# Kernel tuning notes

Measured on AMD Instinct MI355X. Metric: run time of the kernel, lower is better.

The kernel has to match this reference:

```python
import jax, jax.numpy as jnp
import numpy as np

N_HEADS = 16
HEAD_SIZE = 64
N_EMB = 1024
BLOCK = 2048
B, T = 2, 2048

def setup_inputs() -> dict:
    key = jax.random.key(0)
    ks = jax.random.split(key, 6)
    s = 0.02
    x = jax.random.normal(ks[0], (B, T, N_EMB), dtype=jnp.float32)
    # per-head projection weights, stacked: [H, C, hs] (no bias, per module)
    Wq = jax.random.normal(ks[1], (N_HEADS, N_EMB, HEAD_SIZE), dtype=jnp.float32) * s
    Wk = jax.random.normal(ks[2], (N_HEADS, N_EMB, HEAD_SIZE), dtype=jnp.float32) * s
    Wv = jax.random.normal(ks[3], (N_HEADS, N_EMB, HEAD_SIZE), dtype=jnp.float32) * s
    # output projection: Linear(n_heads*head_size -> n_embedding), with bias
    Wo = jax.random.normal(ks[4], (N_HEADS * HEAD_SIZE, N_EMB), dtype=jnp.float32) * s
    bo = jax.random.normal(ks[5], (N_EMB,), dtype=jnp.float32) * s
    return {"x": x, "Wq": Wq, "Wk": Wk, "Wv": Wv, "Wo": Wo, "bo": bo}

def reference(x, Wq, Wk, Wv, Wo, bo):
    # x: [B,T,C]; projections per head -> [B,H,T,hs]
    q = jnp.einsum('btc,hcd->bhtd', x, Wq)
    k = jnp.einsum('btc,hcd->bhtd', x, Wk)
    v = jnp.einsum('btc,hcd->bhtd', x, Wv)
    scale = 1.0 / jnp.sqrt(jnp.asarray(HEAD_SIZE, dtype=x.dtype))
    scores = jnp.einsum('bhtd,bhsd->bhts', q, k) * scale  # [B,H,T,T]
    Tq = x.shape[1]
    causal = jnp.tril(jnp.ones((Tq, Tq), dtype=bool))
    scores = jnp.where(causal, scores, jnp.asarray(-jnp.inf, dtype=scores.dtype))
    attn = jax.nn.softmax(scores, axis=-1)  # dropout in eval mode (identity)
    out = jnp.einsum('bhts,bhsd->bhtd', attn, v)  # [B,H,T,hs]
    # concat heads along last dim (matches torch.cat order over head list)
    out = out.transpose(0, 2, 1, 3).reshape(x.shape[0], Tq, N_HEADS * HEAD_SIZE)
    return out @ Wo + bo
```

## Files before the change

### kernel.cpp

```cpp
#include <hip/hip_runtime.h>


typedef short v8s __attribute__((ext_vector_type(8)));
typedef float v4f __attribute__((ext_vector_type(4)));

#define DEVI __device__ __forceinline__

#define B_SZ 2
#define T_SEQ 2048
#define NH 16
#define HS 64
#define CEMB 1024
#define MROWS (B_SZ * T_SEQ)
#define KSZ 1024
#define SCALE_Q 0.18033688011112042f

DEVI unsigned short f2bf(float f) {
  union { float f; unsigned u; } c; c.f = f;
  unsigned u = c.u;
  unsigned r = (u + 0x7FFFu + ((u >> 16) & 1u)) >> 16;
  return (unsigned short)r;
}

DEVI float exp2_fast(float x) {
  float r;
  asm("v_exp_f32 %0, %1" : "=v"(r) : "v"(x));
  return r;
}

DEVI unsigned cvt_pk_bf16(float lo, float hi) {
  unsigned r;
  asm("v_cvt_pk_bf16_f32 %0, %1, %2" : "=v"(r) : "v"(lo), "v"(hi));
  return r;
}

DEVI void gload_lds16(const void* g, void* l) {
  __builtin_amdgcn_global_load_lds(
      (const __attribute__((address_space(1))) void*)g,
      (__attribute__((address_space(3))) void*)l, 16, 0, 0);
}

DEVI int xcd_swz(int bid, int nwg) {
  int q = nwg >> 3;
  return (bid & 7) * q + (bid >> 3);
}

__global__ __launch_bounds__(256, 4) void prep_kernel(
    const float* __restrict__ x, const float* __restrict__ Wq,
    const float* __restrict__ Wk, const float* __restrict__ Wv,
    const float* __restrict__ Wo, unsigned short* __restrict__ xb,
    unsigned short* __restrict__ Wt, unsigned short* __restrict__ Wot) {
  int bid = blockIdx.x;
  if (bid < 2048) {
    int i = bid * 2048 + threadIdx.x * 8;
    float4 a = *(const float4*)(x + i);
    float4 b = *(const float4*)(x + i + 4);
    ushort4 o0, o1;
    o0.x = f2bf(a.x); o0.y = f2bf(a.y); o0.z = f2bf(a.z); o0.w = f2bf(a.w);
    o1.x = f2bf(b.x); o1.y = f2bf(b.y); o1.z = f2bf(b.z); o1.w = f2bf(b.w);
    *(ushort4*)(xb + i) = o0;
    *(ushort4*)(xb + i + 4) = o1;
    return;
  }
  __shared__ float tile[32][33];
  const float* in; unsigned short* out;
  int C, bx, by;
  if (bid < 5120) {
    int b2 = bid - 2048;
    int widx = b2 >> 10, rem = b2 & 1023;
    in = (widx == 0 ? Wq : (widx == 1 ? Wk : Wv));
    int z = rem >> 6;
    bx = rem & 1; by = (rem >> 1) & 31;
    C = 64;
    in += (size_t)z * 1024 * 64;
    out = Wt + ((size_t)widx << 20) + (size_t)z * 1024 * 64;
  } else {
    int rem = bid - 5120;
    C = 1024;
    bx = rem & 31; by = rem >> 5;
    in = Wo; out = Wot;
  }
  int c0 = bx * 32, r0 = by * 32;
  int tx = threadIdx.x & 31, ty = threadIdx.x >> 5;
#pragma unroll
  for (int j = 0; j < 4; ++j)
    tile[ty + j * 8][tx] = in[(size_t)(r0 + ty + j * 8) * C + c0 + tx];
  __syncthreads();
#pragma unroll
  for (int j = 0; j < 4; ++j)
    out[(size_t)(c0 + ty + j * 8) * 1024 + r0 + tx] = f2bf(tile[tx][ty + j * 8]);
}

template <int MODE>
__global__ __launch_bounds__(256, 3) void gemm_bt(
    const unsigned short* __restrict__ A, const unsigned short* __restrict__ Bt,
    void* __restrict__ Cout, const float* __restrict__ bias, int nbx) {
  __shared__ __align__(16) unsigned char lds[49152];
  unsigned short* As = (unsigned short*)lds;
  unsigned short* Bs = (unsigned short*)(lds + 24576);

  const int tid = threadIdx.x;
  const int lane = tid & 63, w = tid >> 6;
  const int wm = w >> 1, wn = w & 1;
  const int lr = lane & 15, lg = lane >> 4;

  const int wg = xcd_swz(blockIdx.x, gridDim.x);
  const int mb = (wg / nbx) * 128, nb = (wg % nbx) * 128;

  v4f acc[4][4];
  v4f zero = {0.f, 0.f, 0.f, 0.f};
#pragma unroll
  for (int i = 0; i < 4; ++i)
#pragma unroll
    for (int j = 0; j < 4; ++j) acc[i][j] = zero;

  const int srow = lane >> 2;
  const int sgcol = ((lane & 3) ^ (srow & 3)) * 8;
  const unsigned short* gA = A + (size_t)(mb + w * 32 + srow) * KSZ + sgcol;
  const unsigned short* gB = Bt + (size_t)(nb + w * 32 + srow) * KSZ + sgcol;
  unsigned short* lA = As + w * 1024;
  unsigned short* lB = Bs + w * 1024;

#define STAGE_G(buf, kb)                                        \
  do {                                                          \
    gload_lds16(gA + (kb), lA + (buf) * 4096);                  \
    gload_lds16(gA + (kb) + 16 * KSZ, lA + (buf) * 4096 + 512); \
    gload_lds16(gB + (kb), lB + (buf) * 4096);                  \
    gload_lds16(gB + (kb) + 16 * KSZ, lB + (buf) * 4096 + 512); \
  } while (0)

  STAGE_G(0, 0);
  STAGE_G(1, 32);
  STAGE_G(2, 64);

  const int NT = KSZ / 32;
  for (int t = 0; t < NT; ++t) {
    if (t < NT - 2)
      asm volatile("s_waitcnt vmcnt(8)" ::: "memory");
    else if (t == NT - 2)
      asm volatile("s_waitcnt vmcnt(4)" ::: "memory");
    else
      asm volatile("s_waitcnt vmcnt(0)" ::: "memory");
    __builtin_amdgcn_s_barrier();

    const int buf = t % 3;
    v8s af[4], bfr[4];
#pragma unroll
    for (int i = 0; i < 4; ++i) {
      int ra = wm * 64 + i * 16 + lr, rb = wn * 64 + i * 16 + lr;
      af[i]  = *(const v8s*)&As[buf * 4096 + ra * 32 + ((lg ^ (lr & 3)) << 3)];
      bfr[i] = *(const v8s*)&Bs[buf * 4096 + rb * 32 + ((lg ^ (lr & 3)) << 3)];
    }
#pragma unroll
    for (int i = 0; i < 4; ++i)
#pragma unroll
      for (int j = 0; j < 4; ++j)
        acc[i][j] = __builtin_amdgcn_mfma_f32_16x16x32_bf16(af[i], bfr[j], acc[i][j], 0, 0, 0);

    asm volatile("s_waitcnt lgkmcnt(0)" ::: "memory");
    __builtin_amdgcn_s_barrier();
    if (t + 3 < NT) STAGE_G(buf, (t + 3) * 32);
  }
#undef STAGE_G

  if (MODE == 0 && (wg % nbx) >= 16) {
    unsigned short* out = (unsigned short*)Cout;
#pragma unroll
    for (int i = 0; i < 4; ++i) {
      int tl0 = wm * 64 + i * 16 + lg * 4;
      int tc = tl0 >> 3, off = (tl0 & 7) * 2;
#pragma unroll
      for (int j = 0; j < 4; ++j) {
        int dl = wn * 64 + j * 16 + lr;
        unsigned lo = cvt_pk_bf16(acc[i][j][0], acc[i][j][1]);
        unsigned hi = cvt_pk_bf16(acc[i][j][2], acc[i][j][3]);
        unsigned char* p = lds + dl * 256 + ((tc ^ (dl & 15)) << 4) + off;
        *(unsigned*)p = lo;
        *(unsigned*)(p + 4) = hi;
      }
    }
    __syncthreads();
    int b = mb >> 11, mt = mb & 2047;
    int nrem0 = nb & 1023;
    unsigned short* Vg = out + (size_t)(2 * B_SZ * NH) * T_SEQ * HS;
#pragma unroll
    for (int it = 0; it < 8; ++it) {
      int dl = it * 16 + (tid >> 4);
      int tc = tid & 15;
      const unsigned char* p = lds + dl * 256 + ((tc ^ (dl & 15)) << 4);
      int4 vv = *(const int4*)p;
      int nrem = nrem0 + dl;
      int h = nrem >> 6, dd = nrem & 63;
      *(int4*)(Vg + ((size_t)(b * NH + h) * HS + dd) * T_SEQ + mt + tc * 8) = vv;
    }
    return;
  }

#pragma unroll
  for (int i = 0; i < 4; ++i) {
    int mrow0 = mb + wm * 64 + i * 16 + lg * 4;
#pragma unroll
    for (int j = 0; j < 4; ++j) {
      int ncol = nb + wn * 64 + j * 16 + lr;
      if (MODE == 0) {
        int p = ncol >> 10, rem = ncol & 1023, h = rem >> 6, d = rem & 63;
        float sc = (p == 0) ? SCALE_Q : 1.0f;
        unsigned short* out = (unsigned short*)Cout;
#pragma unroll
        for (int r = 0; r < 4; ++r) {
          int mrow = mrow0 + r;
          int b = mrow >> 11, t = mrow & 2047;
          out[((size_t)((p * B_SZ + b) * NH + h) * T_SEQ + t) * HS + d] =
              f2bf(acc[i][j][r] * sc);
        }
      } else {
        float* out = (float*)Cout;
        float bv = bias[ncol];
#pragma unroll
        for (int r = 0; r < 4; ++r)
          out[(size_t)(mrow0 + r) * CEMB + ncol] = acc[i][j][r] + bv;
      }
    }
  }
}

__global__ __launch_bounds__(512, 4) void attn_kernel(
    const unsigned short* __restrict__ Qg, const unsigned short* __restrict__ Kg,
    const unsigned short* __restrict__ Vtg, unsigned short* __restrict__ Yg) {
  __shared__ __align__(16) unsigned char lds[32 * 1024];
  unsigned char* KsB = lds;
  unsigned char* VtB = lds + 16384;

  const int tid = threadIdx.x;
  const int lane = tid & 63, w = tid >> 6;
  const int lr = lane & 15, lg = lane >> 4;
  const int qc = 15 - (blockIdx.x >> 5);
  const int bh = blockIdx.x & 31;

  const unsigned short* Qbase = Qg + (size_t)bh * T_SEQ * HS;
  const unsigned short* Kbase = Kg + (size_t)bh * T_SEQ * HS;
  const unsigned short* Vtbase = Vtg + (size_t)bh * T_SEQ * HS;

  const int ks_row = tid >> 3, ks_cb = tid & 7;
  const int kLds0 = ks_row * 128 + ((ks_cb ^ (ks_row & 7)) << 4);
  const unsigned short* Kg0 = Kbase + ks_row * HS + ks_cb * 8;
  const int vs_d = tid >> 4, vs_m = tid & 15;
  const int vLds0 = vs_d * 256 + ((vs_m ^ (vs_d & 15)) << 4);
  const int vbt = ((vs_m >> 2) << 4) + ((vs_m & 3) << 2);
  const unsigned short* Vg0 = Vtbase + (size_t)vs_d * T_SEQ + vbt;

  v8s qA[2];
  {
    const unsigned short* qrow = Qbase + (size_t)(qc * 128 + w * 16 + lr) * HS;
    qA[0] = *(const v8s*)(qrow + lg * 8);
    qA[1] = *(const v8s*)(qrow + 32 + lg * 8);
  }

  v4f O[4];
  v4f zero = {0.f, 0.f, 0.f, 0.f};
#pragma unroll
  for (int d = 0; d < 4; ++d) O[d] = zero;
  float mrun = -1e30f, lrun = 0.f;

  int4 gK0 = *(const int4*)(Kg0);
  int4 gK1 = *(const int4*)(Kg0 + 4096);
  int2 vlo0 = *(const int2*)(Vg0);
  int2 vhi0 = *(const int2*)(Vg0 + 64);
  int2 vlo1 = *(const int2*)(Vg0 + 32 * T_SEQ);
  int2 vhi1 = *(const int2*)(Vg0 + 32 * T_SEQ + 64);

  for (int t = 0; t <= qc; ++t) {
    __syncthreads();
    *(int4*)(KsB + kLds0) = gK0;
    *(int4*)(KsB + kLds0 + 8192) = gK1;
    {
      int4 v0; v0.x = vlo0.x; v0.y = vlo0.y; v0.z = vhi0.x; v0.w = vhi0.y;
      int4 v1; v1.x = vlo1.x; v1.y = vlo1.y; v1.z = vhi1.x; v1.w = vhi1.y;
      *(int4*)(VtB + vLds0) = v0;
      *(int4*)(VtB + vLds0 + 8192) = v1;
    }
    __syncthreads();
    if (t < qc) {
      const unsigned short* kp = Kg0 + (t + 1) * (128 * HS);
      gK0 = *(const int4*)kp;
      gK1 = *(const int4*)(kp + 4096);
      const unsigned short* vp = Vg0 + (t + 1) * 128;
      vlo0 = *(const int2*)(vp);
      vhi0 = *(const int2*)(vp + 64);
      vlo1 = *(const int2*)(vp + 32 * T_SEQ);
      vhi1 = *(const int2*)(vp + 32 * T_SEQ + 64);
    }

    const int cflim = (t == qc) ? w : 7;

    v4f S[8];
    __builtin_amdgcn_s_setprio(1);
#pragma unroll
    for (int cf = 0; cf < 8; ++cf) {
      if (cf <= cflim) {
        S[cf] = zero;
#pragma unroll
        for (int ks = 0; ks < 2; ++ks) {
          int srow = cf * 16 + lr;
          v8s kb = *(const v8s*)(KsB + srow * 128 +
                                 ((((ks << 2) + lg) ^ (lr & 7)) << 4));
          S[cf] = __builtin_amdgcn_mfma_f32_16x16x32_bf16(kb, qA[ks], S[cf], 0, 0, 0);
        }
      } else {
        S[cf] = (v4f){-1e30f, -1e30f, -1e30f, -1e30f};
      }
    }
    __builtin_amdgcn_s_setprio(0);

    if (t == qc) {
#pragma unroll
      for (int cf = 0; cf < 8; ++cf)
        if (cf == w) {
#pragma unroll
          for (int r = 0; r < 4; ++r)
            if (lg * 4 + r > lr) S[cf][r] = -1e30f;
        }
    }

    float mx = -1e30f;
#pragma unroll
    for (int cf = 0; cf < 8; ++cf)
#pragma unroll
      for (int r = 0; r < 4; ++r) mx = fmaxf(mx, S[cf][r]);
    mx = fmaxf(mx, __shfl_xor(mx, 16));
    mx = fmaxf(mx, __shfl_xor(mx, 32));

    if (!__all(mx - mrun <= 8.0f)) {
      float mn = fmaxf(mrun, mx);
      float alpha = exp2_fast(mrun - mn);
      mrun = mn;
      lrun *= alpha;
#pragma unroll
      for (int df = 0; df < 4; ++df)
#pragma unroll
        for (int r = 0; r < 4; ++r) O[df][r] *= alpha;
    }

    float sum = 0.f;
#pragma unroll
    for (int cf = 0; cf < 8; ++cf)
#pragma unroll
      for (int r = 0; r < 4; ++r) {
        float p = exp2_fast(S[cf][r] - mrun);
        S[cf][r] = p;
        sum += p;
      }
    sum += __shfl_xor(sum, 16);
    sum += __shfl_xor(sum, 32);
    lrun += sum;

    unsigned pk0[8], pk1[8];
#pragma unroll
    for (int cf = 0; cf < 8; ++cf) {
      pk0[cf] = cvt_pk_bf16(S[cf][0], S[cf][1]);
      pk1[cf] = cvt_pk_bf16(S[cf][2], S[cf][3]);
    }

    __builtin_amdgcn_s_setprio(1);
#pragma unroll
    for (int c = 0; c < 4; ++c) {
      if (t != qc || c <= w) {
        union { unsigned u[4]; v8s s; } pu;
        pu.u[0] = pk0[c]; pu.u[1] = pk1[c];
        pu.u[2] = pk0[c + 4]; pu.u[3] = pk1[c + 4];
        v8s pa = pu.s;
#pragma unroll
        for (int df = 0; df < 4; ++df) {
          int d = df * 16 + lr;
          v8s va = *(const v8s*)(VtB + d * 256 +
                                 ((((c << 2) + lg) ^ lr) << 4));
          O[df] = __builtin_amdgcn_mfma_f32_16x16x32_bf16(va, pa, O[df], 0, 0, 0);
        }
      }
    }
    __builtin_amdgcn_s_setprio(0);
  }

  float invl = 1.0f / lrun;
  int tq = qc * 128 + w * 16 + lr;
  int b = bh >> 4, h = bh & 15;
  size_t ybase = ((size_t)b * T_SEQ + tq) * (NH * HS) + h * 64;
#pragma unroll
  for (int df = 0; df < 4; ++df) {
    ushort4 o4;
    o4.x = f2bf(O[df][0] * invl);
    o4.y = f2bf(O[df][1] * invl);
    o4.z = f2bf(O[df][2] * invl);
    o4.w = f2bf(O[df][3] * invl);
    *(ushort4*)(Yg + ybase + df * 16 + lg * 4) = o4;
  }
}

extern "C" void kernel_launch(void* const* d_in, const int* in_sizes, int n_in,
                              void* d_out, int out_size, void* d_ws, size_t ws_size,
                              hipStream_t stream) {
  (void)in_sizes; (void)n_in; (void)out_size; (void)ws_size;
  const float* x  = (const float*)d_in[0];
  const float* Wq = (const float*)d_in[1];
  const float* Wk = (const float*)d_in[2];
  const float* Wv = (const float*)d_in[3];
  const float* Wo = (const float*)d_in[4];
  const float* bo = (const float*)d_in[5];

  unsigned char* ws = (unsigned char*)d_ws;
  unsigned short* xb  = (unsigned short*)(ws);
  unsigned short* Wt  = (unsigned short*)(ws + (8u << 20));
  unsigned short* Wot = (unsigned short*)(ws + (14u << 20));
  unsigned short* qkv = (unsigned short*)(ws + (16u << 20));
  unsigned short* Y   = (unsigned short*)(ws + (40u << 20));

  prep_kernel<<<dim3(6144), 256, 0, stream>>>(x, Wq, Wk, Wv, Wo, xb, Wt, Wot);

  gemm_bt<0><<<dim3(768), 256, 0, stream>>>(xb, Wt, qkv, nullptr, 24);

  const unsigned short* Qp = qkv;
  const unsigned short* Kp = qkv + (size_t)B_SZ * NH * T_SEQ * HS;
  const unsigned short* Vtp = qkv + (size_t)2 * B_SZ * NH * T_SEQ * HS;
  attn_kernel<<<dim3(512), 512, 0, stream>>>(Qp, Kp, Vtp, Y);

  gemm_bt<1><<<dim3(256), 256, 0, stream>>>(Y, Wot, d_out, bo, 8);
}
```

Before: 99.49 us.

## Halve attention query tile and output-projection M tile to raise block count

Attention now uses 64-row query chunks with 256-thread blocks (1024 blocks instead of 512), staging 128-key K/V tiles with wider per-thread loads and handling the diagonal partially for odd chunks. The output projection GEMM gets its own kernel with 64x128 tiles, launching 512 blocks instead of 256, with a smaller triple-buffered LDS footprint. The aim is more concurrent blocks and better load balance across the CUs. The cost is more redundant K/V reloads per query row and lower per-block MFMA reuse.

Result: slower. 111.5 us (+12.1%).

```diff
diff --git a/kernel.cpp b/kernel.cpp
--- a/kernel.cpp
+++ b/kernel.cpp
@@ -91,10 +91,9 @@
     out[(size_t)(c0 + ty + j * 8) * 1024 + r0 + tx] = f2bf(tile[tx][ty + j * 8]);
 }
 
-template <int MODE>
-__global__ __launch_bounds__(256, 3) void gemm_bt(
+__global__ __launch_bounds__(256, 3) void gemm_qkv(
     const unsigned short* __restrict__ A, const unsigned short* __restrict__ Bt,
-    void* __restrict__ Cout, const float* __restrict__ bias, int nbx) {
+    unsigned short* __restrict__ Cout, int nbx) {
   __shared__ __align__(16) unsigned char lds[49152];
   unsigned short* As = (unsigned short*)lds;
   unsigned short* Bs = (unsigned short*)(lds + 24576);
@@ -163,7 +162,7 @@
   }
 #undef STAGE_G
 
-  if (MODE == 0 && (wg % nbx) >= 16) {
+  if ((wg % nbx) >= 16) {
     unsigned short* out = (unsigned short*)Cout;
 #pragma unroll
     for (int i = 0; i < 4; ++i) {
@@ -202,29 +201,108 @@
 #pragma unroll
     for (int j = 0; j < 4; ++j) {
       int ncol = nb + wn * 64 + j * 16 + lr;
-      if (MODE == 0) {
-        int p = ncol >> 10, rem = ncol & 1023, h = rem >> 6, d = rem & 63;
-        float sc = (p == 0) ? SCALE_Q : 1.0f;
-        unsigned short* out = (unsigned short*)Cout;
-#pragma unroll
-        for (int r = 0; r < 4; ++r) {
-          int mrow = mrow0 + r;
-          int b = mrow >> 11, t = mrow & 2047;
-          out[((size_t)((p * B_SZ + b) * NH + h) * T_SEQ + t) * HS + d] =
-              f2bf(acc[i][j][r] * sc);
-        }
-      } else {
-        float* out = (float*)Cout;
-        float bv = bias[ncol];
-#pragma unroll
-        for (int r = 0; r < 4; ++r)
-          out[(size_t)(mrow0 + r) * CEMB + ncol] = acc[i][j][r] + bv;
+      int p = ncol >> 10, rem = ncol & 1023, h = rem >> 6, d = rem & 63;
+      float sc = (p == 0) ? SCALE_Q : 1.0f;
+      unsigned short* out = (unsigned short*)Cout;
+#pragma unroll
+      for (int r = 0; r < 4; ++r) {
+        int mrow = mrow0 + r;
+        int b = mrow >> 11, t = mrow & 2047;
+        out[((size_t)((p * B_SZ + b) * NH + h) * T_SEQ + t) * HS + d] =
+            f2bf(acc[i][j][r] * sc);
       }
     }
   }
 }
 
-__global__ __launch_bounds__(512, 4) void attn_kernel(
+__global__ __launch_bounds__(256, 4) void gemm_proj(
+    const unsigned short* __restrict__ A, const unsigned short* __restrict__ Bt,
+    float* __restrict__ Cout, const float* __restrict__ bias, int nbx) {
+  __shared__ __align__(16) unsigned short As[3][64 * 32];
+  __shared__ __align__(16) unsigned short Bs[3][128 * 32];
+
+  const int tid = threadIdx.x;
+  const int lane = tid & 63, w = tid >> 6;
+  const int wm = w >> 1, wn = w & 1;
+  const int lr = lane & 15, lg = lane >> 4;
+
+  const int wg = xcd_swz(blockIdx.x, gridDim.x);
+  const int mb = (wg / nbx) * 64, nb = (wg % nbx) * 128;
+
+  v4f acc[2][4];
+  v4f zero = {0.f, 0.f, 0.f, 0.f};
+#pragma unroll
+  for (int i = 0; i < 2; ++i)
+#pragma unroll
+    for (int j = 0; j < 4; ++j) acc[i][j] = zero;
+
+  const int srow = lane >> 2;
+  const int sgcol = ((lane & 3) ^ (srow & 3)) * 8;
+  const unsigned short* gA = A + (size_t)(mb + w * 16 + srow) * KSZ + sgcol;
+  const unsigned short* gB = Bt + (size_t)(nb + w * 32 + srow) * KSZ + sgcol;
+  unsigned short* lA = &As[0][0] + w * 512;
+  unsigned short* lB = &Bs[0][0] + w * 1024;
+
+#define STAGE_P(buf, kb)                                        \
+  do {                                                          \
+    gload_lds16(gA + (kb), lA + (buf) * 2048);                  \
+    gload_lds16(gB + (kb), lB + (buf) * 4096);                  \
+    gload_lds16(gB + (kb) + 16 * KSZ, lB + (buf) * 4096 + 512); \
+  } while (0)
+
+  STAGE_P(0, 0);
+  STAGE_P(1, 32);
+  STAGE_P(2, 64);
+
+  const int NT = KSZ / 32;
+  for (int t = 0; t < NT; ++t) {
+    if (t < NT - 2)
+      asm volatile("s_waitcnt vmcnt(6)" ::: "memory");
+    else if (t == NT - 2)
+      asm volatile("s_waitcnt vmcnt(3)" ::: "memory");
+    else
+      asm volatile("s_waitcnt vmcnt(0)" ::: "memory");
+    __builtin_amdgcn_s_barrier();
+
+    const int buf = t % 3;
+    v8s af[2], bfr[4];
+#pragma unroll
+    for (int i = 0; i < 2; ++i) {
+      int ra = wm * 32 + i * 16 + lr;
+      af[i] = *(const v8s*)&As[buf][ra * 32 + ((lg ^ (lr & 3)) << 3)];
+    }
+#pragma unroll
+    for (int j = 0; j < 4; ++j) {
+      int rb = wn * 64 + j * 16 + lr;
+      bfr[j] = *(const v8s*)&Bs[buf][rb * 32 + ((lg ^ (lr & 3)) << 3)];
+    }
+#pragma unroll
+    for (int i = 0; i < 2; ++i)
+#pragma unroll
+      for (int j = 0; j < 4; ++j)
+        acc[i][j] = __builtin_amdgcn_mfma_f32_16x16x32_bf16(af[i], bfr[j], acc[i][j], 0, 0, 0);
+
+    asm volatile("s_waitcnt lgkmcnt(0)" ::: "memory");
+    __builtin_amdgcn_s_barrier();
+    if (t + 3 < NT) STAGE_P(buf, (t + 3) * 32);
+  }
+#undef STAGE_P
+
+#pragma unroll
+  for (int i = 0; i < 2; ++i) {
+    int mrow0 = mb + wm * 32 + i * 16 + lg * 4;
+#pragma unroll
+    for (int j = 0; j < 4; ++j) {
+      int ncol = nb + wn * 64 + j * 16 + lr;
+      float bv = bias[ncol];
+#pragma unroll
+      for (int r = 0; r < 4; ++r)
+        Cout[(size_t)(mrow0 + r) * CEMB + ncol] = acc[i][j][r] + bv;
+    }
+  }
+}
+
+__global__ __launch_bounds__(256, 4) void attn_kernel(
     const unsigned short* __restrict__ Qg, const unsigned short* __restrict__ Kg,
     const unsigned short* __restrict__ Vtg, unsigned short* __restrict__ Yg) {
   __shared__ __align__(16) unsigned char lds[32 * 1024];
@@ -234,24 +312,22 @@
   const int tid = threadIdx.x;
   const int lane = tid & 63, w = tid >> 6;
   const int lr = lane & 15, lg = lane >> 4;
-  const int qc = 15 - (blockIdx.x >> 5);
+  const int qc = 31 - (blockIdx.x >> 5);
   const int bh = blockIdx.x & 31;
 
   const unsigned short* Qbase = Qg + (size_t)bh * T_SEQ * HS;
   const unsigned short* Kbase = Kg + (size_t)bh * T_SEQ * HS;
   const unsigned short* Vtbase = Vtg + (size_t)bh * T_SEQ * HS;
 
-  const int ks_row = tid >> 3, ks_cb = tid & 7;
-  const int kLds0 = ks_row * 128 + ((ks_cb ^ (ks_row & 7)) << 4);
-  const unsigned short* Kg0 = Kbase + ks_row * HS + ks_cb * 8;
-  const int vs_d = tid >> 4, vs_m = tid & 15;
-  const int vLds0 = vs_d * 256 + ((vs_m ^ (vs_d & 15)) << 4);
-  const int vbt = ((vs_m >> 2) << 4) + ((vs_m & 3) << 2);
-  const unsigned short* Vg0 = Vtbase + (size_t)vs_d * T_SEQ + vbt;
+  const int ks_row = tid >> 1, ks_c0 = (tid & 1) * 4;
+  const unsigned short* Kg0 = Kbase + ks_row * HS + ks_c0 * 8;
+  const int vs_d = tid >> 3, m0 = (tid & 7) * 2;
+  const int vbt0 = ((m0 >> 2) << 4) + ((m0 & 3) << 2);
+  const unsigned short* Vg0 = Vtbase + (size_t)vs_d * T_SEQ + vbt0;
 
   v8s qA[2];
   {
-    const unsigned short* qrow = Qbase + (size_t)(qc * 128 + w * 16 + lr) * HS;
+    const unsigned short* qrow = Qbase + (size_t)(qc * 64 + w * 16 + lr) * HS;
     qA[0] = *(const v8s*)(qrow + lg * 8);
     qA[1] = *(const v8s*)(qrow + 32 + lg * 8);
   }
@@ -262,36 +338,47 @@
   for (int d = 0; d < 4; ++d) O[d] = zero;
   float mrun = -1e30f, lrun = 0.f;
 
-  int4 gK0 = *(const int4*)(Kg0);
-  int4 gK1 = *(const int4*)(Kg0 + 4096);
-  int2 vlo0 = *(const int2*)(Vg0);
-  int2 vhi0 = *(const int2*)(Vg0 + 64);
-  int2 vlo1 = *(const int2*)(Vg0 + 32 * T_SEQ);
-  int2 vhi1 = *(const int2*)(Vg0 + 32 * T_SEQ + 64);
-
-  for (int t = 0; t <= qc; ++t) {
+  const int td = qc >> 1, oddq = qc & 1;
+
+  int4 kA0 = ((const int4*)Kg0)[0], kA1 = ((const int4*)Kg0)[1];
+  int4 kA2 = ((const int4*)Kg0)[2], kA3 = ((const int4*)Kg0)[3];
+  int4 vl0 = *(const int4*)(Vg0);
+  int4 vh0 = *(const int4*)(Vg0 + 64);
+  int4 vl1 = *(const int4*)(Vg0 + 32 * T_SEQ);
+  int4 vh1 = *(const int4*)(Vg0 + 32 * T_SEQ + 64);
+
+  for (int t = 0; t <= td; ++t) {
     __syncthreads();
-    *(int4*)(KsB + kLds0) = gK0;
-    *(int4*)(KsB + kLds0 + 8192) = gK1;
     {
-      int4 v0; v0.x = vlo0.x; v0.y = vlo0.y; v0.z = vhi0.x; v0.w = vhi0.y;
-      int4 v1; v1.x = vlo1.x; v1.y = vlo1.y; v1.z = vhi1.x; v1.w = vhi1.y;
-      *(int4*)(VtB + vLds0) = v0;
-      *(int4*)(VtB + vLds0 + 8192) = v1;
+      unsigned char* kp = KsB + ks_row * 128;
+      *(int4*)(kp + (((ks_c0 + 0) ^ (ks_row & 7)) << 4)) = kA0;
+      *(int4*)(kp + (((ks_c0 + 1) ^ (ks_row & 7)) << 4)) = kA1;
+      *(int4*)(kp + (((ks_c0 + 2) ^ (ks_row & 7)) << 4)) = kA2;
+      *(int4*)(kp + (((ks_c0 + 3) ^ (ks_row & 7)) << 4)) = kA3;
+      int4 w0; w0.x = vl0.x; w0.y = vl0.y; w0.z = vh0.x; w0.w = vh0.y;
+      int4 w1; w1.x = vl0.z; w1.y = vl0.w; w1.z = vh0.z; w1.w = vh0.w;
+      unsigned char* vp = VtB + vs_d * 256;
+      *(int4*)(vp + ((m0 ^ (vs_d & 15)) << 4)) = w0;
+      *(int4*)(vp + (((m0 + 1) ^ (vs_d & 15)) << 4)) = w1;
+      int4 w2; w2.x = vl1.x; w2.y = vl1.y; w2.z = vh1.x; w2.w = vh1.y;
+      int4 w3; w3.x = vl1.z; w3.y = vl1.w; w3.z = vh1.z; w3.w = vh1.w;
+      *(int4*)(vp + 8192 + ((m0 ^ (vs_d & 15)) << 4)) = w2;
+      *(int4*)(vp + 8192 + (((m0 + 1) ^ (vs_d & 15)) << 4)) = w3;
     }
     __syncthreads();
-    if (t < qc) {
-      const unsigned short* kp = Kg0 + (t + 1) * (128 * HS);
-      gK0 = *(const int4*)kp;
-      gK1 = *(const int4*)(kp + 4096);
+    if (t < td) {
+      const unsigned short* kp = Kg0 + (t + 1) * 8192;
+      kA0 = ((const int4*)kp)[0]; kA1 = ((const int4*)kp)[1];
+      kA2 = ((const int4*)kp)[2]; kA3 = ((const int4*)kp)[3];
       const unsigned short* vp = Vg0 + (t + 1) * 128;
-      vlo0 = *(const int2*)(vp);
-      vhi0 = *(const int2*)(vp + 64);
-      vlo1 = *(const int2*)(vp + 32 * T_SEQ);
-      vhi1 = *(const int2*)(vp + 32 * T_SEQ + 64);
-    }
-
-    const int cflim = (t == qc) ? w : 7;
+      vl0 = *(const int4*)(vp);
+      vh0 = *(const int4*)(vp + 64);
+      vl1 = *(const int4*)(vp + 32 * T_SEQ);
+      vh1 = *(const int4*)(vp + 32 * T_SEQ + 64);
+    }
+
+    const bool diag = (t == td);
+    const int cflim = diag ? (oddq ? w + 4 : w) : 7;
 
     v4f S[8];
     __builtin_amdgcn_s_setprio(1);
@@ -312,10 +399,10 @@
     }
     __builtin_amdgcn_s_setprio(0);
 
-    if (t == qc) {
+    if (diag) {
 #pragma unroll
       for (int cf = 0; cf < 8; ++cf)
-        if (cf == w) {
+        if (cf == cflim) {
 #pragma unroll
           for (int r = 0; r < 4; ++r)
             if (lg * 4 + r > lr) S[cf][r] = -1e30f;
@@ -364,7 +451,7 @@
     __builtin_amdgcn_s_setprio(1);
 #pragma unroll
     for (int c = 0; c < 4; ++c) {
-      if (t != qc || c <= w) {
+      if (!diag || oddq || c <= w) {
         union { unsigned u[4]; v8s s; } pu;
         pu.u[0] = pk0[c]; pu.u[1] = pk1[c];
         pu.u[2] = pk0[c + 4]; pu.u[3] = pk1[c + 4];
@@ -382,7 +469,7 @@
   }
 
   float invl = 1.0f / lrun;
-  int tq = qc * 128 + w * 16 + lr;
+  int tq = qc * 64 + w * 16 + lr;
   int b = bh >> 4, h = bh & 15;
   size_t ybase = ((size_t)b * T_SEQ + tq) * (NH * HS) + h * 64;
 #pragma unroll
@@ -416,12 +503,12 @@
 
   prep_kernel<<<dim3(6144), 256, 0, stream>>>(x, Wq, Wk, Wv, Wo, xb, Wt, Wot);
 
-  gemm_bt<0><<<dim3(768), 256, 0, stream>>>(xb, Wt, qkv, nullptr, 24);
+  gemm_qkv<<<dim3(768), 256, 0, stream>>>(xb, Wt, qkv, 24);
 
   const unsigned short* Qp = qkv;
   const unsigned short* Kp = qkv + (size_t)B_SZ * NH * T_SEQ * HS;
   const unsigned short* Vtp = qkv + (size_t)2 * B_SZ * NH * T_SEQ * HS;
-  attn_kernel<<<dim3(512), 512, 0, stream>>>(Qp, Kp, Vtp, Y);
-
-  gemm_bt<1><<<dim3(256), 256, 0, stream>>>(Y, Wot, d_out, bo, 8);
-}
+  attn_kernel<<<dim3(1024), 256, 0, stream>>>(Qp, Kp, Vtp, Y);
+
+  gemm_proj<<<dim3(512), 256, 0, stream>>>(Y, Wot, (float*)d_out, bo, 8);
+}
```

## Double-buffer K/V tiles in LDS to drop one barrier per iteration

Applied to the files above, without the earlier changes.

The attention kernel now keeps two LDS buffers for the K and V tiles, 64KB in total, and prefetches registers two tiles ahead. The next tile is written into the alternate buffer while the current one is consumed, so each iteration needs one __syncthreads instead of two. In exchange, launch bounds drop from 4 to 2 blocks per CU and LDS use doubles, which lowers occupancy.

Result: no change. 99.61 us (+0.1%).

```diff
diff --git a/kernel.cpp b/kernel.cpp
--- a/kernel.cpp
+++ b/kernel.cpp
@@ -224,12 +224,10 @@
   }
 }
 
-__global__ __launch_bounds__(512, 4) void attn_kernel(
+__global__ __launch_bounds__(512, 2) void attn_kernel(
     const unsigned short* __restrict__ Qg, const unsigned short* __restrict__ Kg,
     const unsigned short* __restrict__ Vtg, unsigned short* __restrict__ Yg) {
-  __shared__ __align__(16) unsigned char lds[32 * 1024];
-  unsigned char* KsB = lds;
-  unsigned char* VtB = lds + 16384;
+  __shared__ __align__(16) unsigned char lds[64 * 1024];
 
   const int tid = threadIdx.x;
   const int lane = tid & 63, w = tid >> 6;
@@ -262,34 +260,45 @@
   for (int d = 0; d < 4; ++d) O[d] = zero;
   float mrun = -1e30f, lrun = 0.f;
 
-  int4 gK0 = *(const int4*)(Kg0);
-  int4 gK1 = *(const int4*)(Kg0 + 4096);
-  int2 vlo0 = *(const int2*)(Vg0);
-  int2 vhi0 = *(const int2*)(Vg0 + 64);
-  int2 vlo1 = *(const int2*)(Vg0 + 32 * T_SEQ);
-  int2 vhi1 = *(const int2*)(Vg0 + 32 * T_SEQ + 64);
+  int4 gK0, gK1;
+  int2 vlo0, vhi0, vlo1, vhi1;
+
+#define LOAD_REGS(tt)                                         \
+  do {                                                        \
+    const unsigned short* kp = Kg0 + (tt) * (128 * HS);       \
+    gK0 = *(const int4*)kp;                                   \
+    gK1 = *(const int4*)(kp + 4096);                          \
+    const unsigned short* vp = Vg0 + (tt) * 128;              \
+    vlo0 = *(const int2*)(vp);                                \
+    vhi0 = *(const int2*)(vp + 64);                           \
+    vlo1 = *(const int2*)(vp + 32 * T_SEQ);                   \
+    vhi1 = *(const int2*)(vp + 32 * T_SEQ + 64);              \
+  } while (0)
+
+#define WRITE_BUF(bsel)                                               \
+  do {                                                                \
+    unsigned char* kb_ = lds + (bsel) * 16384;                        \
+    unsigned char* vb_ = lds + 32768 + (bsel) * 16384;                \
+    *(int4*)(kb_ + kLds0) = gK0;                                      \
+    *(int4*)(kb_ + kLds0 + 8192) = gK1;                               \
+    int4 v0_; v0_.x = vlo0.x; v0_.y = vlo0.y; v0_.z = vhi0.x; v0_.w = vhi0.y; \
+    int4 v1_; v1_.x = vlo1.x; v1_.y = vlo1.y; v1_.z = vhi1.x; v1_.w = vhi1.y; \
+    *(int4*)(vb_ + vLds0) = v0_;                                      \
+    *(int4*)(vb_ + vLds0 + 8192) = v1_;                               \
+  } while (0)
+
+  LOAD_REGS(0);
+  WRITE_BUF(0);
+  if (qc >= 1) LOAD_REGS(1);
 
   for (int t = 0; t <= qc; ++t) {
     __syncthreads();
-    *(int4*)(KsB + kLds0) = gK0;
-    *(int4*)(KsB + kLds0 + 8192) = gK1;
-    {
-      int4 v0; v0.x = vlo0.x; v0.y = vlo0.y; v0.z = vhi0.x; v0.w = vhi0.y;
-      int4 v1; v1.x = vlo1.x; v1.y = vlo1.y; v1.z = vhi1.x; v1.w = vhi1.y;
-      *(int4*)(VtB + vLds0) = v0;
-      *(int4*)(VtB + vLds0 + 8192) = v1;
-    }
-    __syncthreads();
     if (t < qc) {
-      const unsigned short* kp = Kg0 + (t + 1) * (128 * HS);
-      gK0 = *(const int4*)kp;
-      gK1 = *(const int4*)(kp + 4096);
-      const unsigned short* vp = Vg0 + (t + 1) * 128;
-      vlo0 = *(const int2*)(vp);
-      vhi0 = *(const int2*)(vp + 64);
-      vlo1 = *(const int2*)(vp + 32 * T_SEQ);
-      vhi1 = *(const int2*)(vp + 32 * T_SEQ + 64);
-    }
+      WRITE_BUF((t + 1) & 1);
+      if (t + 2 <= qc) LOAD_REGS(t + 2);
+    }
+    const unsigned char* KsB = lds + (t & 1) * 16384;
+    const unsigned char* VtB = lds + 32768 + (t & 1) * 16384;
 
     const int cflim = (t == qc) ? w : 7;
 
@@ -380,6 +389,8 @@
     }
     __builtin_amdgcn_s_setprio(0);
   }
+#undef LOAD_REGS
+#undef WRITE_BUF
 
   float invl = 1.0f / lrun;
   int tq = qc * 128 + w * 16 + lr;
```

## Process two query row groups per wave in attention to reuse K/V fragments

Applied to the files above, without the earlier changes.

The attention kernel drops from 8 waves to 4 waves per 128-row query tile. Each wave now handles two 16-row query groups, keeping separate softmax state and output accumulators for each. Every K and V fragment read from shared memory feeds two MFMAs instead of one, which halves LDS traffic per unit of compute, and each thread stages twice as many global loads. In exchange, register pressure rises, there are fewer waves to hide latency, and the skipping of masked MFMAs on the diagonal tile is removed, so some redundant work is now computed and then masked.

Result: slower. 116.1 us (+16.7%).

```diff
diff --git a/kernel.cpp b/kernel.cpp
--- a/kernel.cpp
+++ b/kernel.cpp
@@ -224,7 +224,7 @@
   }
 }
 
-__global__ __launch_bounds__(512, 4) void attn_kernel(
+__global__ __launch_bounds__(256, 2) void attn_kernel(
     const unsigned short* __restrict__ Qg, const unsigned short* __restrict__ Kg,
     const unsigned short* __restrict__ Vtg, unsigned short* __restrict__ Yg) {
   __shared__ __align__(16) unsigned char lds[32 * 1024];
@@ -249,150 +249,200 @@
   const int vbt = ((vs_m >> 2) << 4) + ((vs_m & 3) << 2);
   const unsigned short* Vg0 = Vtbase + (size_t)vs_d * T_SEQ + vbt;
 
-  v8s qA[2];
+  v8s qA0[2], qA1[2];
   {
-    const unsigned short* qrow = Qbase + (size_t)(qc * 128 + w * 16 + lr) * HS;
-    qA[0] = *(const v8s*)(qrow + lg * 8);
-    qA[1] = *(const v8s*)(qrow + 32 + lg * 8);
-  }
-
-  v4f O[4];
+    const unsigned short* q0 = Qbase + (size_t)(qc * 128 + w * 16 + lr) * HS;
+    qA0[0] = *(const v8s*)(q0 + lg * 8);
+    qA0[1] = *(const v8s*)(q0 + 32 + lg * 8);
+    const unsigned short* q1 = q0 + 64 * HS;
+    qA1[0] = *(const v8s*)(q1 + lg * 8);
+    qA1[1] = *(const v8s*)(q1 + 32 + lg * 8);
+  }
+
   v4f zero = {0.f, 0.f, 0.f, 0.f};
-#pragma unroll
-  for (int d = 0; d < 4; ++d) O[d] = zero;
-  float mrun = -1e30f, lrun = 0.f;
-
-  int4 gK0 = *(const int4*)(Kg0);
-  int4 gK1 = *(const int4*)(Kg0 + 4096);
-  int2 vlo0 = *(const int2*)(Vg0);
-  int2 vhi0 = *(const int2*)(Vg0 + 64);
-  int2 vlo1 = *(const int2*)(Vg0 + 32 * T_SEQ);
-  int2 vhi1 = *(const int2*)(Vg0 + 32 * T_SEQ + 64);
+  v4f neg4 = {-1e30f, -1e30f, -1e30f, -1e30f};
+  v4f O0[4], O1[4];
+#pragma unroll
+  for (int d = 0; d < 4; ++d) { O0[d] = zero; O1[d] = zero; }
+  float m0 = -1e30f, l0 = 0.f, m1 = -1e30f, l1 = 0.f;
+
+  int4 kK[4];
+  int2 vl[4], vh[4];
+#pragma unroll
+  for (int k = 0; k < 4; ++k) {
+    kK[k] = *(const int4*)(Kg0 + k * 2048);
+    vl[k] = *(const int2*)(Vg0 + k * 16 * T_SEQ);
+    vh[k] = *(const int2*)(Vg0 + k * 16 * T_SEQ + 64);
+  }
 
   for (int t = 0; t <= qc; ++t) {
     __syncthreads();
-    *(int4*)(KsB + kLds0) = gK0;
-    *(int4*)(KsB + kLds0 + 8192) = gK1;
-    {
-      int4 v0; v0.x = vlo0.x; v0.y = vlo0.y; v0.z = vhi0.x; v0.w = vhi0.y;
-      int4 v1; v1.x = vlo1.x; v1.y = vlo1.y; v1.z = vhi1.x; v1.w = vhi1.y;
-      *(int4*)(VtB + vLds0) = v0;
-      *(int4*)(VtB + vLds0 + 8192) = v1;
+#pragma unroll
+    for (int k = 0; k < 4; ++k) {
+      *(int4*)(KsB + kLds0 + k * 4096) = kK[k];
+      int4 wv; wv.x = vl[k].x; wv.y = vl[k].y; wv.z = vh[k].x; wv.w = vh[k].y;
+      *(int4*)(VtB + vLds0 + k * 4096) = wv;
     }
     __syncthreads();
     if (t < qc) {
-      const unsigned short* kp = Kg0 + (t + 1) * (128 * HS);
-      gK0 = *(const int4*)kp;
-      gK1 = *(const int4*)(kp + 4096);
+      const unsigned short* kp = Kg0 + (t + 1) * 8192;
       const unsigned short* vp = Vg0 + (t + 1) * 128;
-      vlo0 = *(const int2*)(vp);
-      vhi0 = *(const int2*)(vp + 64);
-      vlo1 = *(const int2*)(vp + 32 * T_SEQ);
-      vhi1 = *(const int2*)(vp + 32 * T_SEQ + 64);
-    }
-
-    const int cflim = (t == qc) ? w : 7;
-
-    v4f S[8];
+#pragma unroll
+      for (int k = 0; k < 4; ++k) {
+        kK[k] = *(const int4*)(kp + k * 2048);
+        vl[k] = *(const int2*)(vp + k * 16 * T_SEQ);
+        vh[k] = *(const int2*)(vp + k * 16 * T_SEQ + 64);
+      }
+    }
+
+    v4f S0[8], S1[8];
     __builtin_amdgcn_s_setprio(1);
 #pragma unroll
     for (int cf = 0; cf < 8; ++cf) {
-      if (cf <= cflim) {
-        S[cf] = zero;
-#pragma unroll
-        for (int ks = 0; ks < 2; ++ks) {
-          int srow = cf * 16 + lr;
-          v8s kb = *(const v8s*)(KsB + srow * 128 +
-                                 ((((ks << 2) + lg) ^ (lr & 7)) << 4));
-          S[cf] = __builtin_amdgcn_mfma_f32_16x16x32_bf16(kb, qA[ks], S[cf], 0, 0, 0);
+      int srow = cf * 16 + lr;
+      v8s kb0 = *(const v8s*)(KsB + srow * 128 + ((lg ^ (lr & 7)) << 4));
+      v8s kb1 = *(const v8s*)(KsB + srow * 128 + (((4 + lg) ^ (lr & 7)) << 4));
+      v4f s0 = __builtin_amdgcn_mfma_f32_16x16x32_bf16(kb0, qA0[0], zero, 0, 0, 0);
+      S0[cf]  = __builtin_amdgcn_mfma_f32_16x16x32_bf16(kb1, qA0[1], s0, 0, 0, 0);
+      v4f s1 = __builtin_amdgcn_mfma_f32_16x16x32_bf16(kb0, qA1[0], zero, 0, 0, 0);
+      S1[cf]  = __builtin_amdgcn_mfma_f32_16x16x32_bf16(kb1, qA1[1], s1, 0, 0, 0);
+    }
+    __builtin_amdgcn_s_setprio(0);
+
+    if (t == qc) {
+#pragma unroll
+      for (int cf = 0; cf < 8; ++cf) {
+        if (cf == w) {
+#pragma unroll
+          for (int r = 0; r < 4; ++r)
+            if (lg * 4 + r > lr) S0[cf][r] = -1e30f;
+        } else if (cf > w) {
+          S0[cf] = neg4;
         }
-      } else {
-        S[cf] = (v4f){-1e30f, -1e30f, -1e30f, -1e30f};
+        if (cf == 4 + w) {
+#pragma unroll
+          for (int r = 0; r < 4; ++r)
+            if (lg * 4 + r > lr) S1[cf][r] = -1e30f;
+        } else if (cf > 4 + w) {
+          S1[cf] = neg4;
+        }
+      }
+    }
+
+    {
+      float mx = -1e30f;
+#pragma unroll
+      for (int cf = 0; cf < 8; ++cf)
+#pragma unroll
+        for (int r = 0; r < 4; ++r) mx = fmaxf(mx, S0[cf][r]);
+      mx = fmaxf(mx, __shfl_xor(mx, 16));
+      mx = fmaxf(mx, __shfl_xor(mx, 32));
+      if (!__all(mx - m0 <= 8.0f)) {
+        float mn = fmaxf(m0, mx);
+        float alpha = exp2_fast(m0 - mn);
+        m0 = mn;
+        l0 *= alpha;
+#pragma unroll
+        for (int df = 0; df < 4; ++df)
+#pragma unroll
+          for (int r = 0; r < 4; ++r) O0[df][r] *= alpha;
+      }
+      float sum = 0.f;
+#pragma unroll
+      for (int cf = 0; cf < 8; ++cf)
+#pragma unroll
+        for (int r = 0; r < 4; ++r) {
+          float p = exp2_fast(S0[cf][r] - m0);
+          S0[cf][r] = p;
+          sum += p;
+        }
+      sum += __shfl_xor(sum, 16);
+      sum += __shfl_xor(sum, 32);
+      l0 += sum;
+    }
+    {
+      float mx = -1e30f;
+#pragma unroll
+      for (int cf = 0; cf < 8; ++cf)
+#pragma unroll
+        for (int r = 0; r < 4; ++r) mx = fmaxf(mx, S1[cf][r]);
+      mx = fmaxf(mx, __shfl_xor(mx, 16));
+      mx = fmaxf(mx, __shfl_xor(mx, 32));
+      if (!__all(mx - m1 <= 8.0f)) {
+        float mn = fmaxf(m1, mx);
+        float alpha = exp2_fast(m1 - mn);
+        m1 = mn;
+        l1 *= alpha;
+#pragma unroll
+        for (int df = 0; df < 4; ++df)
+#pragma unroll
+          for (int r = 0; r < 4; ++r) O1[df][r] *= alpha;
+      }
+      float sum = 0.f;
+#pragma unroll
+      for (int cf = 0; cf < 8; ++cf)
+#pragma unroll
+        for (int r = 0; r < 4; ++r) {
+          float p = exp2_fast(S1[cf][r] - m1);
+          S1[cf][r] = p;
+          sum += p;
+        }
+      sum += __shfl_xor(sum, 16);
+      sum += __shfl_xor(sum, 32);
+      l1 += sum;
+    }
+
+    __builtin_amdgcn_s_setprio(1);
+#pragma unroll
+    for (int c = 0; c < 4; ++c) {
+      union { unsigned u[4]; v8s s; } p0, p1;
+      p0.u[0] = cvt_pk_bf16(S0[c][0], S0[c][1]);
+      p0.u[1] = cvt_pk_bf16(S0[c][2], S0[c][3]);
+      p0.u[2] = cvt_pk_bf16(S0[c + 4][0], S0[c + 4][1]);
+      p0.u[3] = cvt_pk_bf16(S0[c + 4][2], S0[c + 4][3]);
+      p1.u[0] = cvt_pk_bf16(S1[c][0], S1[c][1]);
+      p1.u[1] = cvt_pk_bf16(S1[c][2], S1[c][3]);
+      p1.u[2] = cvt_pk_bf16(S1[c + 4][0], S1[c + 4][1]);
+      p1.u[3] = cvt_pk_bf16(S1[c + 4][2], S1[c + 4][3]);
+#pragma unroll
+      for (int df = 0; df < 4; ++df) {
+        int d = df * 16 + lr;
+        v8s va = *(const v8s*)(VtB + d * 256 + ((((c << 2) + lg) ^ lr) << 4));
+        O0[df] = __builtin_amdgcn_mfma_f32_16x16x32_bf16(va, p0.s, O0[df], 0, 0, 0);
+        O1[df] = __builtin_amdgcn_mfma_f32_16x16x32_bf16(va, p1.s, O1[df], 0, 0, 0);
       }
     }
     __builtin_amdgcn_s_setprio(0);
-
-    if (t == qc) {
-#pragma unroll
-      for (int cf = 0; cf < 8; ++cf)
-        if (cf == w) {
-#pragma unroll
-          for (int r = 0; r < 4; ++r)
-            if (lg * 4 + r > lr) S[cf][r] = -1e30f;
-        }
-    }
-
-    float mx = -1e30f;
-#pragma unroll
-    for (int cf = 0; cf < 8; ++cf)
-#pragma unroll
-      for (int r = 0; r < 4; ++r) mx = fmaxf(mx, S[cf][r]);
-    mx = fmaxf(mx, __shfl_xor(mx, 16));
-    mx = fmaxf(mx, __shfl_xor(mx, 32));
-
-    if (!__all(mx - mrun <= 8.0f)) {
-      float mn = fmaxf(mrun, mx);
-      float alpha = exp2_fast(mrun - mn);
-      mrun = mn;
-      lrun *= alpha;
-#pragma unroll
-      for (int df = 0; df < 4; ++df)
-#pragma unroll
-        for (int r = 0; r < 4; ++r) O[df][r] *= alpha;
-    }
-
-    float sum = 0.f;
-#pragma unroll
-    for (int cf = 0; cf < 8; ++cf)
-#pragma unroll
-      for (int r = 0; r < 4; ++r) {
-        float p = exp2_fast(S[cf][r] - mrun);
-        S[cf][r] = p;
-        sum += p;
-      }
-    sum += __shfl_xor(sum, 16);
-    sum += __shfl_xor(sum, 32);
-    lrun += sum;
-
-    unsigned pk0[8], pk1[8];
-#pragma unroll
-    for (int cf = 0; cf < 8; ++cf) {
-      pk0[cf] = cvt_pk_bf16(S[cf][0], S[cf][1]);
-      pk1[cf] = cvt_pk_bf16(S[cf][2], S[cf][3]);
-    }
-
-    __builtin_amdgcn_s_setprio(1);
-#pragma unroll
-    for (int c = 0; c < 4; ++c) {
-      if (t != qc || c <= w) {
-        union { unsigned u[4]; v8s s; } pu;
-        pu.u[0] = pk0[c]; pu.u[1] = pk1[c];
-        pu.u[2] = pk0[c + 4]; pu.u[3] = pk1[c + 4];
-        v8s pa = pu.s;
-#pragma unroll
-        for (int df = 0; df < 4; ++df) {
-          int d = df * 16 + lr;
-          v8s va = *(const v8s*)(VtB + d * 256 +
-                                 ((((c << 2) + lg) ^ lr) << 4));
-          O[df] = __builtin_amdgcn_mfma_f32_16x16x32_bf16(va, pa, O[df], 0, 0, 0);
-        }
-      }
-    }
-    __builtin_amdgcn_s_setprio(0);
-  }
-
-  float invl = 1.0f / lrun;
-  int tq = qc * 128 + w * 16 + lr;
+  }
+
   int b = bh >> 4, h = bh & 15;
-  size_t ybase = ((size_t)b * T_SEQ + tq) * (NH * HS) + h * 64;
-#pragma unroll
-  for (int df = 0; df < 4; ++df) {
-    ushort4 o4;
-    o4.x = f2bf(O[df][0] * invl);
-    o4.y = f2bf(O[df][1] * invl);
-    o4.z = f2bf(O[df][2] * invl);
-    o4.w = f2bf(O[df][3] * invl);
-    *(ushort4*)(Yg + ybase + df * 16 + lg * 4) = o4;
+  {
+    float invl = 1.0f / l0;
+    int tq = qc * 128 + w * 16 + lr;
+    size_t ybase = ((size_t)b * T_SEQ + tq) * (NH * HS) + h * 64;
+#pragma unroll
+    for (int df = 0; df < 4; ++df) {
+      ushort4 o4;
+      o4.x = f2bf(O0[df][0] * invl);
+      o4.y = f2bf(O0[df][1] * invl);
+      o4.z = f2bf(O0[df][2] * invl);
+      o4.w = f2bf(O0[df][3] * invl);
+      *(ushort4*)(Yg + ybase + df * 16 + lg * 4) = o4;
+    }
+  }
+  {
+    float invl = 1.0f / l1;
+    int tq = qc * 128 + 64 + w * 16 + lr;
+    size_t ybase = ((size_t)b * T_SEQ + tq) * (NH * HS) + h * 64;
+#pragma unroll
+    for (int df = 0; df < 4; ++df) {
+      ushort4 o4;
+      o4.x = f2bf(O1[df][0] * invl);
+      o4.y = f2bf(O1[df][1] * invl);
+      o4.z = f2bf(O1[df][2] * invl);
+      o4.w = f2bf(O1[df][3] * invl);
+      *(ushort4*)(Yg + ybase + df * 16 + lg * 4) = o4;
+    }
   }
 }
 
@@ -421,7 +471,7 @@
   const unsigned short* Qp = qkv;
   const unsigned short* Kp = qkv + (size_t)B_SZ * NH * T_SEQ * HS;
   const unsigned short* Vtp = qkv + (size_t)2 * B_SZ * NH * T_SEQ * HS;
-  attn_kernel<<<dim3(512), 512, 0, stream>>>(Qp, Kp, Vtp, Y);
+  attn_kernel<<<dim3(512), 256, 0, stream>>>(Qp, Kp, Vtp, Y);
 
   gemm_bt<1><<<dim3(256), 256, 0, stream>>>(Y, Wot, d_out, bo, 8);
 }
```
